# Performance work log

Measured on AMD Instinct MI355X. Metric: run time of the kernel, lower is better.

## Reference

```python
import jax, jax.numpy as jnp
import numpy as np

DIM = 64
HID = 64
BATCH = 16384
L = DIM - 1  # number of FCNN layers (for dims 1..DIM-1)


def setup_inputs() -> dict:
    key = jax.random.key(0)
    ks = jax.random.split(key, 8)
    bound = float(np.sqrt(0.5))
    return {
        "x": jax.random.normal(ks[0], (BATCH, DIM), jnp.float32),
        "initial_param": jax.random.uniform(ks[1], (2,), jnp.float32, -bound, bound),
        # padded per-layer weights: layer l uses input columns 0..l only (masked in reference)
        "W1": jax.random.normal(ks[2], (L, L, HID), jnp.float32) * 0.1,
        "b1": jnp.zeros((L, HID), jnp.float32),
        "W2": jax.random.normal(ks[3], (L, HID, HID), jnp.float32) * 0.1,
        "b2": jnp.zeros((L, HID), jnp.float32),
        "W3": jax.random.normal(ks[4], (L, HID, 2), jnp.float32) * 0.1,
        "b3": jnp.zeros((L, 2), jnp.float32),
    }


def reference(x, initial_param, W1, b1, W2, b2, W3, b3):
    B = x.shape[0]
    # mask[l, j] = 1 if input column j is visible to layer l (layer l == FCNN(in_dim=l+1))
    mask = (jnp.arange(L)[None, :] <= jnp.arange(L)[:, None]).astype(x.dtype)  # [L, L]
    xin = x[:, :L]                                                             # [B, L]
    # all per-dim FCNNs in one batched pass (equivalent to the Python loop over x[:, :i])
    h1 = jnp.tanh(jnp.einsum('bj,ljh->blh', xin, W1 * mask[:, :, None]) + b1)  # [B, L, H]
    h2 = jnp.tanh(jnp.einsum('blh,lhk->blk', h1, W2) + b2)                     # [B, L, H]
    out = jnp.einsum('blh,lhk->blk', h2, W3) + b3                              # [B, L, 2]
    mu0 = jnp.full((B, 1), initial_param[0], x.dtype)
    a0 = jnp.full((B, 1), initial_param[1], x.dtype)
    mu = jnp.concatenate([mu0, out[..., 0]], axis=1)      # [B, DIM]
    alpha = jnp.concatenate([a0, out[..., 1]], axis=1)    # [B, DIM]
    z = (x - mu) * jnp.exp(-alpha)
    log_det = -jnp.sum(alpha, axis=1)                     # [B]
    return z[:, ::-1], log_det
```

## Files before the change

### kernel.cpp

```cpp
#include <hip/hip_runtime.h>

#define LN 63
#define BATCHN 16384

typedef __attribute__((ext_vector_type(8))) short bf16x8;
typedef __attribute__((ext_vector_type(4))) float f32x4;

__device__ __forceinline__ float fast_exp(float v) {
    return __builtin_amdgcn_exp2f(v * 1.4426950408889634f);
}
__device__ __forceinline__ float fast_tanh(float v) {
    float e = __builtin_amdgcn_exp2f(v * 2.8853900817779268f);
    return 1.0f - 2.0f * __builtin_amdgcn_rcpf(e + 1.0f);
}
__device__ __forceinline__ short f2bf(float f) {
    __bf16 h = (__bf16)f;
    return __builtin_bit_cast(short, h);
}
__device__ __forceinline__ unsigned int pk2(float a, float b) {
    return (unsigned int)(unsigned short)f2bf(a) |
           ((unsigned int)(unsigned short)f2bf(b) << 16);
}

__device__ __forceinline__ int kappa_j(int s, int g, int e) {
    return (e < 4) ? (32 * s + 4 * g + e) : (32 * s + 16 + 4 * g + e - 4);
}

__global__ __launch_bounds__(256) void prep_kernel(
    const float* __restrict__ x,
    const float* __restrict__ W1, const float* __restrict__ b1,
    const float* __restrict__ W2, const float* __restrict__ W3,
    unsigned short* __restrict__ Afrag,
    unsigned short* __restrict__ xbf)
{
    const int t = threadIdx.x;
    const int b = blockIdx.x;
    if (b >= LN) {
        const int i = ((b - LN) * 256 + t) * 4;
        const float4 v = *reinterpret_cast<const float4*>(x + i);
        ushort4 o;
        o.x = (unsigned short)f2bf(v.x);
        o.y = (unsigned short)f2bf(v.y);
        o.z = (unsigned short)f2bf(v.z);
        o.w = (unsigned short)f2bf(v.w);
        *reinterpret_cast<ushort4*>(xbf + i) = o;
        return;
    }
    const int l = b;
    unsigned short* Af = Afrag + (size_t)l * 9216;

    #pragma unroll
    for (int it = 0; it < 2; ++it) {
        const int item = t + it * 256;
        const int s = item >> 8, tt = (item >> 6) & 3, lane = item & 63;
        const int g = lane >> 4, mcol = lane & 15, h = 16 * tt + mcol;
        unsigned pk[4];
        #pragma unroll
        for (int ep = 0; ep < 4; ++ep) {
            float v[2];
            #pragma unroll
            for (int k = 0; k < 2; ++k) {
                const int e = 2 * ep + k;
                const int j = 32 * s + 8 * g + e;
                float val;
                if (j == 63)      val = b1[l * 64 + h];
                else if (j <= l)  val = W1[(l * LN + j) * 64 + h];
                else              val = 0.0f;
                v[k] = val;
            }
            pk[ep] = pk2(v[0], v[1]);
        }
        *reinterpret_cast<uint4*>(Af + ((size_t)item) * 8) =
            uint4{pk[0], pk[1], pk[2], pk[3]};
    }
    #pragma unroll
    for (int it = 0; it < 2; ++it) {
        const int item = t + it * 256;
        const int s = item >> 8, tt = (item >> 6) & 3, lane = item & 63;
        const int g = lane >> 4, mcol = lane & 15, h = 16 * tt + mcol;
        unsigned pk[4];
        #pragma unroll
        for (int ep = 0; ep < 4; ++ep) {
            float v[2];
            #pragma unroll
            for (int k = 0; k < 2; ++k) {
                const int e = 2 * ep + k;
                v[k] = W2[(l * 64 + kappa_j(s, g, e)) * 64 + h];
            }
            pk[ep] = pk2(v[0], v[1]);
        }
        *reinterpret_cast<uint4*>(Af + 4096 + ((size_t)item) * 8) =
            uint4{pk[0], pk[1], pk[2], pk[3]};
    }
    if (t < 128) {
        const int s = t >> 6, lane = t & 63;
        const int g = lane >> 4, mcol = lane & 15;
        unsigned pk[4] = {0u, 0u, 0u, 0u};
        if (mcol < 2) {
            #pragma unroll
            for (int ep = 0; ep < 4; ++ep) {
                float v[2];
                #pragma unroll
                for (int k = 0; k < 2; ++k) {
                    const int e = 2 * ep + k;
                    v[k] = W3[(l * 64 + kappa_j(s, g, e)) * 2 + mcol];
                }
                pk[ep] = pk2(v[0], v[1]);
            }
        }
        *reinterpret_cast<uint4*>(Af + 8192 + ((size_t)t) * 8) =
            uint4{pk[0], pk[1], pk[2], pk[3]};
    }
}

struct ChainOut { float mu, al; };

template<int XBF>
__global__ __launch_bounds__(256, 2) void maf_main_kernel(
    const float* __restrict__ x,
    const unsigned short* __restrict__ xbf,
    const unsigned short* __restrict__ Afrag,
    const float* __restrict__ b2,
    const float* __restrict__ b3,
    float* __restrict__ zT,
    float* __restrict__ aT)
{
    const int t = threadIdx.x;
    const int bid = blockIdx.x;
    const int l = bid % LN;
    const int rowBase = (bid / LN) * 1024;

    const int lane = t & 63;
    const int w = t >> 6;
    const int g = lane >> 4;
    const int mcol = lane & 15;

    const unsigned short* Af = Afrag + (size_t)l * 9216;
    bf16x8 w2f[2][4], w3f[2];
    #pragma unroll
    for (int s = 0; s < 2; ++s) {
        #pragma unroll
        for (int tt = 0; tt < 4; ++tt)
            w2f[s][tt] = *reinterpret_cast<const bf16x8*>(Af + 4096 + ((s * 4 + tt) * 64 + lane) * 8);
        w3f[s] = *reinterpret_cast<const bf16x8*>(Af + 8192 + (s * 64 + lane) * 8);
    }
    f32x4 bias2[4];
    #pragma unroll
    for (int tt = 0; tt < 4; ++tt) {
        const float4 v2 = *reinterpret_cast<const float4*>(&b2[l * 64 + 16 * tt + 4 * g]);
        bias2[tt] = f32x4{v2.x, v2.y, v2.z, v2.w};
    }
    const float b30 = b3[l * 2 + 0];
    const float b31 = b3[l * 2 + 1];
    const short one_bf = (short)0x3F80;

    const int rowW = rowBase + w * 256 + mcol;
    const unsigned short* xrow = xbf + (size_t)rowW * 64 + 8 * g;

    auto ldxf = [&](int k, bf16x8& f0, bf16x8& f1) {
        const unsigned short* p = xrow + (size_t)(16 * k) * 64;
        f0 = *reinterpret_cast<const bf16x8*>(p);
        f1 = *reinterpret_cast<const bf16x8*>(p + 32);
        if (g == 3) f1[7] = one_bf;
    };

    bf16x8 xa0, xa1, xb0, xb1, na0, na1, nb0, nb1;
    ldxf(0, xa0, xa1);
    ldxf(1, xb0, xb1);

    #pragma unroll 1
    for (int it = 0; it < 8; ++it) {
        const int nk = (it < 7) ? (2 * it + 2) : 14;
        ldxf(nk, na0, na1);
        ldxf(nk + 1, nb0, nb1);

        bf16x8 w1f[2][4];
        #pragma unroll
        for (int s = 0; s < 2; ++s)
            #pragma unroll
            for (int tt = 0; tt < 4; ++tt)
                w1f[s][tt] = *reinterpret_cast<const bf16x8*>(Af + ((s * 4 + tt) * 64 + lane) * 8);

        f32x4 c1a[4], c1b[4];
        #pragma unroll
        for (int tt = 0; tt < 4; ++tt) {
            c1a[tt] = f32x4{0.0f, 0.0f, 0.0f, 0.0f};
            c1b[tt] = f32x4{0.0f, 0.0f, 0.0f, 0.0f};
        }
        #pragma unroll
        for (int tt = 0; tt < 4; ++tt) {
            c1a[tt] = __builtin_amdgcn_mfma_f32_16x16x32_bf16(w1f[0][tt], xa0, c1a[tt], 0, 0, 0);
            c1b[tt] = __builtin_amdgcn_mfma_f32_16x16x32_bf16(w1f[0][tt], xb0, c1b[tt], 0, 0, 0);
        }
        #pragma unroll
        for (int tt = 0; tt < 4; ++tt) {
            c1a[tt] = __builtin_amdgcn_mfma_f32_16x16x32_bf16(w1f[1][tt], xa1, c1a[tt], 0, 0, 0);
            c1b[tt] = __builtin_amdgcn_mfma_f32_16x16x32_bf16(w1f[1][tt], xb1, c1b[tt], 0, 0, 0);
        }

        bf16x8 pfa[2], pfb[2];
        #pragma unroll
        for (int s = 0; s < 2; ++s) {
            bf16x8 fa, fb;
            #pragma unroll
            for (int q = 0; q < 4; ++q) {
                fa[q]     = f2bf(fast_tanh(c1a[2 * s][q]));
                fb[q]     = f2bf(fast_tanh(c1b[2 * s][q]));
                fa[4 + q] = f2bf(fast_tanh(c1a[2 * s + 1][q]));
                fb[4 + q] = f2bf(fast_tanh(c1b[2 * s + 1][q]));
            }
            pfa[s] = fa;
            pfb[s] = fb;
        }

        f32x4 c2a[4], c2b[4];
        #pragma unroll
        for (int tt = 0; tt < 4; ++tt) { c2a[tt] = bias2[tt]; c2b[tt] = bias2[tt]; }
        #pragma unroll
        for (int s = 0; s < 2; ++s)
            #pragma unroll
            for (int tt = 0; tt < 4; ++tt) {
                c2a[tt] = __builtin_amdgcn_mfma_f32_16x16x32_bf16(w2f[s][tt], pfa[s], c2a[tt], 0, 0, 0);
                c2b[tt] = __builtin_amdgcn_mfma_f32_16x16x32_bf16(w2f[s][tt], pfb[s], c2b[tt], 0, 0, 0);
            }

        bf16x8 qfa[2], qfb[2];
        #pragma unroll
        for (int s = 0; s < 2; ++s) {
            bf16x8 fa, fb;
            #pragma unroll
            for (int q = 0; q < 4; ++q) {
                fa[q]     = f2bf(fast_tanh(c2a[2 * s][q]));
                fb[q]     = f2bf(fast_tanh(c2b[2 * s][q]));
                fa[4 + q] = f2bf(fast_tanh(c2a[2 * s + 1][q]));
                fb[4 + q] = f2bf(fast_tanh(c2b[2 * s + 1][q]));
            }
            qfa[s] = fa;
            qfb[s] = fb;
        }

        f32x4 c3a = {0.0f, 0.0f, 0.0f, 0.0f};
        f32x4 c3b = {0.0f, 0.0f, 0.0f, 0.0f};
        c3a = __builtin_amdgcn_mfma_f32_16x16x32_bf16(w3f[0], qfa[0], c3a, 0, 0, 0);
        c3b = __builtin_amdgcn_mfma_f32_16x16x32_bf16(w3f[0], qfb[0], c3b, 0, 0, 0);
        c3a = __builtin_amdgcn_mfma_f32_16x16x32_bf16(w3f[1], qfa[1], c3a, 0, 0, 0);
        c3b = __builtin_amdgcn_mfma_f32_16x16x32_bf16(w3f[1], qfb[1], c3b, 0, 0, 0);

        if (g == 0) {
            const int rowA = rowW + 32 * it;
            const int rowB = rowA + 16;
            const float muA = c3a[0] + b30, alA = c3a[1] + b31;
            const float muB = c3b[0] + b30, alB = c3b[1] + b31;
            const float xnA = x[(size_t)rowA * 64 + l + 1];
            const float xnB = x[(size_t)rowB * 64 + l + 1];
            zT[(62 - l) * BATCHN + rowA] = (xnA - muA) * fast_exp(-alA);
            zT[(62 - l) * BATCHN + rowB] = (xnB - muB) * fast_exp(-alB);
            aT[l * BATCHN + rowA] = alA;
            aT[l * BATCHN + rowB] = alB;
        }

        xa0 = na0; xa1 = na1; xb0 = nb0; xb1 = nb1;
    }
}

__global__ __launch_bounds__(256) void maf_finish_kernel(
    const float* __restrict__ x,
    const float* __restrict__ ip,
    const float* __restrict__ zT,
    const float* __restrict__ aT,
    float* __restrict__ z_out,
    float* __restrict__ ld_out)
{
    __shared__ float tile[64][65];

    const int t = threadIdx.x;
    const int rb = blockIdx.x * 64;
    const float mu0 = ip[0];
    const float a0  = ip[1];
    const float e0  = fast_exp(-a0);

    {
        const int r = t >> 2, c = t & 3;
        const int row = rb + r;
        float s = 0.0f;
        for (int i = c; i < LN; i += 4) s += aT[(size_t)i * BATCHN + row];
        s += __shfl_xor(s, 1, 64);
        s += __shfl_xor(s, 2, 64);
        if (c == 0) ld_out[row] = -(s + a0);
    }

    const int r = t & 63, cq = t >> 6;
    #pragma unroll
    for (int k = 0; k < 16; ++k) {
        const int c = cq * 16 + k;
        float v;
        if (c < 63) v = zT[(size_t)c * BATCHN + rb + r];
        else        v = (x[(size_t)(rb + r) * 64] - mu0) * e0;
        tile[c][r] = v;
    }
    __syncthreads();
    #pragma unroll
    for (int i = 0; i < 16; ++i) {
        const int rr = cq * 16 + i;
        z_out[(size_t)(rb + rr) * 64 + r] = tile[r][rr];
    }
}

extern "C" void kernel_launch(void* const* d_in, const int* in_sizes, int n_in,
                              void* d_out, int out_size, void* d_ws, size_t ws_size,
                              hipStream_t stream) {
    const float* x  = (const float*)d_in[0];
    const float* ip = (const float*)d_in[1];
    const float* W1 = (const float*)d_in[2];
    const float* b1 = (const float*)d_in[3];
    const float* W2 = (const float*)d_in[4];
    const float* b2 = (const float*)d_in[5];
    const float* W3 = (const float*)d_in[6];
    const float* b3 = (const float*)d_in[7];

    float* z_out  = (float*)d_out;
    float* ld_out = z_out + (size_t)BATCHN * 64;

    unsigned short* Afrag = (unsigned short*)d_ws;
    float* zT = (float*)((char*)d_ws + (size_t)LN * 9216 * 2);
    float* aT = zT + (size_t)LN * BATCHN;
    unsigned short* xbf = (unsigned short*)(aT + (size_t)LN * BATCHN);

    prep_kernel<<<dim3(LN + BATCHN * 64 / 1024), dim3(256), 0, stream>>>(
        x, W1, b1, W2, W3, Afrag, xbf);
    maf_main_kernel<1><<<dim3(LN * 16), dim3(256), 0, stream>>>(
        x, xbf, Afrag, b2, b3, zT, aT);
    maf_finish_kernel<<<dim3(BATCHN / 64), dim3(256), 0, stream>>>(
        x, ip, zT, aT, z_out, ld_out);
}
```

Measured before the change: 65.62 us.

## Switch MLP to fp16 MFMA with packed rational tanh approximation

```diff
diff --git a/kernel.cpp b/kernel.cpp
--- a/kernel.cpp
+++ b/kernel.cpp
@@ -1,25 +1,42 @@
 #include <hip/hip_runtime.h>
+#include <hip/hip_fp16.h>
 
 #define LN 63
 #define BATCHN 16384
 
-typedef __attribute__((ext_vector_type(8))) short bf16x8;
+typedef _Float16 f16x8 __attribute__((ext_vector_type(8)));
+typedef _Float16 h2    __attribute__((ext_vector_type(2)));
 typedef __attribute__((ext_vector_type(4))) float f32x4;
 
 __device__ __forceinline__ float fast_exp(float v) {
     return __builtin_amdgcn_exp2f(v * 1.4426950408889634f);
 }
-__device__ __forceinline__ float fast_tanh(float v) {
-    float e = __builtin_amdgcn_exp2f(v * 2.8853900817779268f);
-    return 1.0f - 2.0f * __builtin_amdgcn_rcpf(e + 1.0f);
-}
-__device__ __forceinline__ short f2bf(float f) {
-    __bf16 h = (__bf16)f;
-    return __builtin_bit_cast(short, h);
-}
-__device__ __forceinline__ unsigned int pk2(float a, float b) {
-    return (unsigned int)(unsigned short)f2bf(a) |
-           ((unsigned int)(unsigned short)f2bf(b) << 16);
+__device__ __forceinline__ unsigned short f2h(float f) {
+    _Float16 h = (_Float16)f;
+    return __builtin_bit_cast(unsigned short, h);
+}
+__device__ __forceinline__ unsigned int pk2h(float a, float b) {
+    return (unsigned int)f2h(a) | ((unsigned int)f2h(b) << 16);
+}
+
+__device__ __forceinline__ h2 tanh_pk(float a, float b) {
+    const h2 c945 = {(_Float16)945.0f, (_Float16)945.0f};
+    const h2 c105 = {(_Float16)105.0f, (_Float16)105.0f};
+    const h2 c420 = {(_Float16)420.0f, (_Float16)420.0f};
+    const h2 c15  = {(_Float16)15.0f,  (_Float16)15.0f};
+    const h2 clim = {(_Float16)4.5f,   (_Float16)4.5f};
+    const h2 cone = {(_Float16)1.0f,   (_Float16)1.0f};
+    h2 v = __builtin_bit_cast(h2, __builtin_amdgcn_cvt_pkrtz(a, b));
+    v = __builtin_elementwise_min(v, clim);
+    v = __builtin_elementwise_max(v, -clim);
+    h2 v2  = v * v;
+    h2 num = v * (v2 * (v2 + c105) + c945);
+    h2 den = v2 * (v2 * c15 + c420) + c945;
+    __half2 r = h2rcp(__builtin_bit_cast(__half2, den));
+    h2 res = num * __builtin_bit_cast(h2, r);
+    res = __builtin_elementwise_min(res, cone);
+    res = __builtin_elementwise_max(res, -cone);
+    return res;
 }
 
 __device__ __forceinline__ int kappa_j(int s, int g, int e) {
@@ -31,7 +48,7 @@
     const float* __restrict__ W1, const float* __restrict__ b1,
     const float* __restrict__ W2, const float* __restrict__ W3,
     unsigned short* __restrict__ Afrag,
-    unsigned short* __restrict__ xbf)
+    unsigned short* __restrict__ xh)
 {
     const int t = threadIdx.x;
     const int b = blockIdx.x;
@@ -39,11 +56,8 @@
         const int i = ((b - LN) * 256 + t) * 4;
         const float4 v = *reinterpret_cast<const float4*>(x + i);
         ushort4 o;
-        o.x = (unsigned short)f2bf(v.x);
-        o.y = (unsigned short)f2bf(v.y);
-        o.z = (unsigned short)f2bf(v.z);
-        o.w = (unsigned short)f2bf(v.w);
-        *reinterpret_cast<ushort4*>(xbf + i) = o;
+        o.x = f2h(v.x); o.y = f2h(v.y); o.z = f2h(v.z); o.w = f2h(v.w);
+        *reinterpret_cast<ushort4*>(xh + i) = o;
         return;
     }
     const int l = b;
@@ -68,7 +82,7 @@
                 else              val = 0.0f;
                 v[k] = val;
             }
-            pk[ep] = pk2(v[0], v[1]);
+            pk[ep] = pk2h(v[0], v[1]);
         }
         *reinterpret_cast<uint4*>(Af + ((size_t)item) * 8) =
             uint4{pk[0], pk[1], pk[2], pk[3]};
@@ -87,7 +101,7 @@
                 const int e = 2 * ep + k;
                 v[k] = W2[(l * 64 + kappa_j(s, g, e)) * 64 + h];
             }
-            pk[ep] = pk2(v[0], v[1]);
+            pk[ep] = pk2h(v[0], v[1]);
         }
         *reinterpret_cast<uint4*>(Af + 4096 + ((size_t)item) * 8) =
             uint4{pk[0], pk[1], pk[2], pk[3]};
@@ -105,7 +119,7 @@
                     const int e = 2 * ep + k;
                     v[k] = W3[(l * 64 + kappa_j(s, g, e)) * 2 + mcol];
                 }
-                pk[ep] = pk2(v[0], v[1]);
+                pk[ep] = pk2h(v[0], v[1]);
             }
         }
         *reinterpret_cast<uint4*>(Af + 8192 + ((size_t)t) * 8) =
@@ -113,12 +127,9 @@
     }
 }
 
-struct ChainOut { float mu, al; };
-
-template<int XBF>
 __global__ __launch_bounds__(256, 2) void maf_main_kernel(
     const float* __restrict__ x,
-    const unsigned short* __restrict__ xbf,
+    const unsigned short* __restrict__ xh,
     const unsigned short* __restrict__ Afrag,
     const float* __restrict__ b2,
     const float* __restrict__ b3,
@@ -136,13 +147,15 @@
     const int mcol = lane & 15;
 
     const unsigned short* Af = Afrag + (size_t)l * 9216;
-    bf16x8 w2f[2][4], w3f[2];
+    f16x8 w1f[2][4], w2f[2][4], w3f[2];
     #pragma unroll
     for (int s = 0; s < 2; ++s) {
         #pragma unroll
-        for (int tt = 0; tt < 4; ++tt)
-            w2f[s][tt] = *reinterpret_cast<const bf16x8*>(Af + 4096 + ((s * 4 + tt) * 64 + lane) * 8);
-        w3f[s] = *reinterpret_cast<const bf16x8*>(Af + 8192 + (s * 64 + lane) * 8);
+        for (int tt = 0; tt < 4; ++tt) {
+            w1f[s][tt] = *reinterpret_cast<const f16x8*>(Af + ((s * 4 + tt) * 64 + lane) * 8);
+            w2f[s][tt] = *reinterpret_cast<const f16x8*>(Af + 4096 + ((s * 4 + tt) * 64 + lane) * 8);
+        }
+        w3f[s] = *reinterpret_cast<const f16x8*>(Af + 8192 + (s * 64 + lane) * 8);
     }
     f32x4 bias2[4];
     #pragma unroll
@@ -152,21 +165,22 @@
     }
     const float b30 = b3[l * 2 + 0];
     const float b31 = b3[l * 2 + 1];
-    const short one_bf = (short)0x3F80;
 
     const int rowW = rowBase + w * 256 + mcol;
-    const unsigned short* xrow = xbf + (size_t)rowW * 64 + 8 * g;
-
-    auto ldxf = [&](int k, bf16x8& f0, bf16x8& f1) {
+    const unsigned short* xrow = xh + (size_t)rowW * 64 + 8 * g;
+
+    auto ldxf = [&](int k, f16x8& f0, f16x8& f1) {
         const unsigned short* p = xrow + (size_t)(16 * k) * 64;
-        f0 = *reinterpret_cast<const bf16x8*>(p);
-        f1 = *reinterpret_cast<const bf16x8*>(p + 32);
-        if (g == 3) f1[7] = one_bf;
+        f0 = *reinterpret_cast<const f16x8*>(p);
+        f1 = *reinterpret_cast<const f16x8*>(p + 32);
+        if (g == 3) f1[7] = (_Float16)1.0f;
     };
 
-    bf16x8 xa0, xa1, xb0, xb1, na0, na1, nb0, nb1;
+    f16x8 xa0, xa1, xb0, xb1, na0, na1, nb0, nb1;
     ldxf(0, xa0, xa1);
     ldxf(1, xb0, xb1);
+
+    union U8 { h2 d[4]; f16x8 v; };
 
     #pragma unroll 1
     for (int it = 0; it < 8; ++it) {
@@ -174,13 +188,6 @@
         ldxf(nk, na0, na1);
         ldxf(nk + 1, nb0, nb1);
 
-        bf16x8 w1f[2][4];
-        #pragma unroll
-        for (int s = 0; s < 2; ++s)
-            #pragma unroll
-            for (int tt = 0; tt < 4; ++tt)
-                w1f[s][tt] = *reinterpret_cast<const bf16x8*>(Af + ((s * 4 + tt) * 64 + lane) * 8);
-
         f32x4 c1a[4], c1b[4];
         #pragma unroll
         for (int tt = 0; tt < 4; ++tt) {
@@ -189,28 +196,29 @@
         }
         #pragma unroll
         for (int tt = 0; tt < 4; ++tt) {
-            c1a[tt] = __builtin_amdgcn_mfma_f32_16x16x32_bf16(w1f[0][tt], xa0, c1a[tt], 0, 0, 0);
-            c1b[tt] = __builtin_amdgcn_mfma_f32_16x16x32_bf16(w1f[0][tt], xb0, c1b[tt], 0, 0, 0);
+            c1a[tt] = __builtin_amdgcn_mfma_f32_16x16x32_f16(w1f[0][tt], xa0, c1a[tt], 0, 0, 0);
+            c1b[tt] = __builtin_amdgcn_mfma_f32_16x16x32_f16(w1f[0][tt], xb0, c1b[tt], 0, 0, 0);
         }
         #pragma unroll
         for (int tt = 0; tt < 4; ++tt) {
-            c1a[tt] = __builtin_amdgcn_mfma_f32_16x16x32_bf16(w1f[1][tt], xa1, c1a[tt], 0, 0, 0);
-            c1b[tt] = __builtin_amdgcn_mfma_f32_16x16x32_bf16(w1f[1][tt], xb1, c1b[tt], 0, 0, 0);
-        }
-
-        bf16x8 pfa[2], pfb[2];
+            c1a[tt] = __builtin_amdgcn_mfma_f32_16x16x32_f16(w1f[1][tt], xa1, c1a[tt], 0, 0, 0);
+            c1b[tt] = __builtin_amdgcn_mfma_f32_16x16x32_f16(w1f[1][tt], xb1, c1b[tt], 0, 0, 0);
+        }
+
+        f16x8 pfa[2], pfb[2];
         #pragma unroll
         for (int s = 0; s < 2; ++s) {
-            bf16x8 fa, fb;
-            #pragma unroll
-            for (int q = 0; q < 4; ++q) {
-                fa[q]     = f2bf(fast_tanh(c1a[2 * s][q]));
-                fb[q]     = f2bf(fast_tanh(c1b[2 * s][q]));
-                fa[4 + q] = f2bf(fast_tanh(c1a[2 * s + 1][q]));
-                fb[4 + q] = f2bf(fast_tanh(c1b[2 * s + 1][q]));
-            }
-            pfa[s] = fa;
-            pfb[s] = fb;
+            U8 ua, ub;
+            ua.d[0] = tanh_pk(c1a[2 * s][0], c1a[2 * s][1]);
+            ub.d[0] = tanh_pk(c1b[2 * s][0], c1b[2 * s][1]);
+            ua.d[1] = tanh_pk(c1a[2 * s][2], c1a[2 * s][3]);
+            ub.d[1] = tanh_pk(c1b[2 * s][2], c1b[2 * s][3]);
+            ua.d[2] = tanh_pk(c1a[2 * s + 1][0], c1a[2 * s + 1][1]);
+            ub.d[2] = tanh_pk(c1b[2 * s + 1][0], c1b[2 * s + 1][1]);
+            ua.d[3] = tanh_pk(c1a[2 * s + 1][2], c1a[2 * s + 1][3]);
+            ub.d[3] = tanh_pk(c1b[2 * s + 1][2], c1b[2 * s + 1][3]);
+            pfa[s] = ua.v;
+            pfb[s] = ub.v;
         }
 
         f32x4 c2a[4], c2b[4];
@@ -220,31 +228,32 @@
         for (int s = 0; s < 2; ++s)
             #pragma unroll
             for (int tt = 0; tt < 4; ++tt) {
-                c2a[tt] = __builtin_amdgcn_mfma_f32_16x16x32_bf16(w2f[s][tt], pfa[s], c2a[tt], 0, 0, 0);
-                c2b[tt] = __builtin_amdgcn_mfma_f32_16x16x32_bf16(w2f[s][tt], pfb[s], c2b[tt], 0, 0, 0);
+                c2a[tt] = __builtin_amdgcn_mfma_f32_16x16x32_f16(w2f[s][tt], pfa[s], c2a[tt], 0, 0, 0);
+                c2b[tt] = __builtin_amdgcn_mfma_f32_16x16x32_f16(w2f[s][tt], pfb[s], c2b[tt], 0, 0, 0);
             }
 
-        bf16x8 qfa[2], qfb[2];
+        f16x8 qfa[2], qfb[2];
         #pragma unroll
         for (int s = 0; s < 2; ++s) {
-            bf16x8 fa, fb;
-            #pragma unroll
-            for (int q = 0; q < 4; ++q) {
-                fa[q]     = f2bf(fast_tanh(c2a[2 * s][q]));
-                fb[q]     = f2bf(fast_tanh(c2b[2 * s][q]));
-                fa[4 + q] = f2bf(fast_tanh(c2a[2 * s + 1][q]));
-                fb[4 + q] = f2bf(fast_tanh(c2b[2 * s + 1][q]));
-            }
-            qfa[s] = fa;
-            qfb[s] = fb;
+            U8 ua, ub;
+            ua.d[0] = tanh_pk(c2a[2 * s][0], c2a[2 * s][1]);
+            ub.d[0] = tanh_pk(c2b[2 * s][0], c2b[2 * s][1]);
+            ua.d[1] = tanh_pk(c2a[2 * s][2], c2a[2 * s][3]);
+            ub.d[1] = tanh_pk(c2b[2 * s][2], c2b[2 * s][3]);
+            ua.d[2] = tanh_pk(c2a[2 * s + 1][0], c2a[2 * s + 1][1]);
+            ub.d[2] = tanh_pk(c2b[2 * s + 1][0], c2b[2 * s + 1][1]);
+            ua.d[3] = tanh_pk(c2a[2 * s + 1][2], c2a[2 * s + 1][3]);
+            ub.d[3] = tanh_pk(c2b[2 * s + 1][2], c2b[2 * s + 1][3]);
+            qfa[s] = ua.v;
+            qfb[s] = ub.v;
         }
 
         f32x4 c3a = {0.0f, 0.0f, 0.0f, 0.0f};
         f32x4 c3b = {0.0f, 0.0f, 0.0f, 0.0f};
-        c3a = __builtin_amdgcn_mfma_f32_16x16x32_bf16(w3f[0], qfa[0], c3a, 0, 0, 0);
-        c3b = __builtin_amdgcn_mfma_f32_16x16x32_bf16(w3f[0], qfb[0], c3b, 0, 0, 0);
-        c3a = __builtin_amdgcn_mfma_f32_16x16x32_bf16(w3f[1], qfa[1], c3a, 0, 0, 0);
-        c3b = __builtin_amdgcn_mfma_f32_16x16x32_bf16(w3f[1], qfb[1], c3b, 0, 0, 0);
+        c3a = __builtin_amdgcn_mfma_f32_16x16x32_f16(w3f[0], qfa[0], c3a, 0, 0, 0);
+        c3b = __builtin_amdgcn_mfma_f32_16x16x32_f16(w3f[0], qfb[0], c3b, 0, 0, 0);
+        c3a = __builtin_amdgcn_mfma_f32_16x16x32_f16(w3f[1], qfa[1], c3a, 0, 0, 0);
+        c3b = __builtin_amdgcn_mfma_f32_16x16x32_f16(w3f[1], qfb[1], c3b, 0, 0, 0);
 
         if (g == 0) {
             const int rowA = rowW + 32 * it;
@@ -324,12 +333,12 @@
     unsigned short* Afrag = (unsigned short*)d_ws;
     float* zT = (float*)((char*)d_ws + (size_t)LN * 9216 * 2);
     float* aT = zT + (size_t)LN * BATCHN;
-    unsigned short* xbf = (unsigned short*)(aT + (size_t)LN * BATCHN);
+    unsigned short* xh = (unsigned short*)(aT + (size_t)LN * BATCHN);
 
     prep_kernel<<<dim3(LN + BATCHN * 64 / 1024), dim3(256), 0, stream>>>(
-        x, W1, b1, W2, W3, Afrag, xbf);
-    maf_main_kernel<1><<<dim3(LN * 16), dim3(256), 0, stream>>>(
-        x, xbf, Afrag, b2, b3, zT, aT);
+        x, W1, b1, W2, W3, Afrag, xh);
+    maf_main_kernel<<<dim3(LN * 16), dim3(256), 0, stream>>>(
+        x, xh, Afrag, b2, b3, zT, aT);
     maf_finish_kernel<<<dim3(BATCHN / 64), dim3(256), 0, stream>>>(
         x, ip, zT, aT, z_out, ld_out);
 }
```

Result: slower. 70.96 us (+8.1%).
